# Performance work log

Hardware: AMD Instinct MI355X
Metric: run time of the kernel (lower is better)

## Reference

```python
import jax, jax.numpy as jnp
import numpy as np

H = 512  # hidden size

def _lstm_layer(xseq, W_ih, W_hh, b_ih, b_hh):
    """xseq: [S,B,D]. Returns (h_seq [S,B,H], c_final [B,H]). PyTorch gate order i,f,g,o."""
    S, B, _ = xseq.shape
    # precompute input contribution for all timesteps: [S,B,4H]
    gx = jnp.einsum('sbd,gd->sbg', xseq, W_ih) + b_ih + b_hh
    h0 = jnp.zeros((B, H), xseq.dtype)
    c0 = jnp.zeros((B, H), xseq.dtype)

    def step(carry, gx_t):
        h, c = carry
        gates = gx_t + h @ W_hh.T  # [B,4H]
        i, f, g, o = jnp.split(gates, 4, axis=-1)
        c = jax.nn.sigmoid(f) * c + jax.nn.sigmoid(i) * jnp.tanh(g)
        h = jax.nn.sigmoid(o) * jnp.tanh(c)
        return (h, c), h

    (_, c_fin), h_seq = jax.lax.scan(step, (h0, c0), gx)
    return h_seq, c_fin


def setup_inputs() -> dict:
    key = jax.random.key(0)
    ks = jax.random.split(key, 12)
    V, D, L = 50257, 300, 10
    s = 0.08  # weight scale to keep gates in a sane range
    return {
        'x': jax.random.randint(ks[0], (64, 512), 0, V),
        'emb': jax.random.normal(ks[1], (V, D), jnp.float32),
        'W_ih0': s * jax.random.normal(ks[2], (4 * H, D), jnp.float32),
        'W_hh0': s * jax.random.normal(ks[3], (4 * H, H), jnp.float32),
        'b_ih0': s * jax.random.normal(ks[4], (4 * H,), jnp.float32),
        'b_hh0': s * jax.random.normal(ks[5], (4 * H,), jnp.float32),
        'W_ih1': s * jax.random.normal(ks[6], (4 * H, H), jnp.float32),
        'W_hh1': s * jax.random.normal(ks[7], (4 * H, H), jnp.float32),
        'b_ih1': s * jax.random.normal(ks[8], (4 * H,), jnp.float32),
        'b_hh1': s * jax.random.normal(ks[9], (4 * H,), jnp.float32),
        'W_out': s * jax.random.normal(ks[10], (L, H), jnp.float32),
        'b_out': s * jax.random.normal(ks[11], (L,), jnp.float32),
    }


def reference(x, emb, W_ih0, W_hh0, b_ih0, b_hh0, W_ih1, W_hh1, b_ih1, b_hh1, W_out, b_out):
    xe = emb[x]                      # [B,S,D] embedding gather
    xe = jnp.transpose(xe, (1, 0, 2))  # [S,B,D] time-major for scan
    h1, _ = _lstm_layer(xe, W_ih0, W_hh0, b_ih0, b_hh0)
    _, c2 = _lstm_layer(h1, W_ih1, W_hh1, b_ih1, b_hh1)  # c_n[-1]: [B,H]
    return c2 @ W_out.T + b_out      # [B,n_labels]
```

## Files before the change

### kernel.cpp

```cpp
#include <hip/hip_runtime.h>
#include <hip/hip_bf16.h>
#include <stdint.h>

#define BB 64
#define SS 512
#define HH 512
#define DD 300
#define DP 320

typedef __attribute__((ext_vector_type(8))) short short8;
typedef __attribute__((ext_vector_type(4))) float f32x4;

__device__ __forceinline__ unsigned short f2bf(float f) {
  unsigned u = __builtin_bit_cast(unsigned, f);
  u += 0x7fffu + ((u >> 16) & 1u);
  return (unsigned short)(u >> 16);
}
__device__ __forceinline__ float sigm(float x) { return 1.f / (1.f + __expf(-x)); }
__device__ __forceinline__ float tanh_f(float x) {
  float t = __expf(-2.f * fabsf(x));
  float r = (1.f - t) / (1.f + t);
  return x < 0.f ? -r : r;
}

__device__ __forceinline__ short8 load_frag_sc1(const unsigned short* p) {
  short8 r;
  asm volatile("global_load_dwordx4 %0, %1, off sc1" : "=v"(r) : "v"(p));
  return r;
}
__device__ __forceinline__ short8 load_frag(const unsigned short* p) {
  short8 r;
  asm volatile("global_load_dwordx4 %0, %1, off" : "=v"(r) : "v"(p));
  return r;
}

#define OFF_ARR   0u
#define OFF_EP    8192u
#define OFF_H1    16384u
#define OFF_H2    147456u
#define OFF_C2    278528u
#define OFF_XE    409600u
#define OFF_W0    21381120u
#define OFF_W1    24788992u
#define OFF_B0    28983296u
#define OFF_B1    28991488u
#define MEMSET_BYTES 278528u

__global__ void prep_weights(const float* __restrict__ Wih0, const float* __restrict__ Whh0,
                             const float* __restrict__ bih0, const float* __restrict__ bhh0,
                             const float* __restrict__ Wih1, const float* __restrict__ Whh1,
                             const float* __restrict__ bih1, const float* __restrict__ bhh1,
                             unsigned short* __restrict__ Wp0, unsigned short* __restrict__ Wp1,
                             float* __restrict__ b0p, float* __restrict__ b1p)
{
  int idx = blockIdx.x * 256 + threadIdx.x;
  int grow = idx >> 10;
  int k1 = idx & 1023;
  int l = grow & 31;
  int lb = grow >> 5;
  int gate = l >> 3;
  int orig = gate * 512 + lb * 8 + (l & 7);
  float v1 = (k1 < 512) ? Wih1[orig * 512 + k1] : Whh1[orig * 512 + (k1 - 512)];
  Wp1[idx] = f2bf(v1);
  if (k1 < 832) {
    float v0;
    if (k1 < 512)      v0 = Whh0[orig * 512 + k1];
    else if (k1 < 812) v0 = Wih0[orig * 300 + (k1 - 512)];
    else               v0 = 0.f;
    Wp0[grow * 832 + k1] = f2bf(v0);
  }
  if (k1 == 0) {
    b0p[grow] = bih0[orig] + bhh0[orig];
    b1p[grow] = bih1[orig] + bhh1[orig];
  }
}

__global__ void gather_xe(const int* __restrict__ x, const float* __restrict__ emb,
                          unsigned short* __restrict__ xe)
{
  int idx = blockIdx.x * 256 + threadIdx.x;
  int dk = idx % DP;
  int rem = idx / DP;
  int b = rem % BB;
  int t = rem / BB;
  int tok = x[b * SS + t];
  float v = (dk < DD) ? emb[(size_t)tok * DD + dk] : 0.f;
  size_t ua = (size_t)t * 20480 + (size_t)(dk >> 5) * 2048 + (size_t)(b >> 4) * 512
            + (size_t)((dk >> 3) & 3) * 128 + (size_t)(b & 15) * 8 + (dk & 7);
  xe[ua] = f2bf(v);
}

template<bool IS_L0>
__device__ __forceinline__ void scan_body(
    int blk,
    const unsigned short* __restrict__ xe,
    const unsigned short* __restrict__ Wp,
    const float* __restrict__ biasP,
    unsigned short* __restrict__ h1r,
    unsigned short* __restrict__ h2r,
    float* __restrict__ c2,
    unsigned int* cnt,
    float (&gl)[2][64][36], float (&bias_sm)[32])
{
  constexpr int K  = IS_L0 ? 832 : 1024;
  constexpr int NK = IS_L0 ? 13 : 16;

  const int tid  = threadIdx.x;
  const int lane = tid & 63;
  const int wave = tid >> 6;
  const int lrow = lane & 15;
  const int m    = wave & 3;
  const int q    = wave >> 2;
  const int lblk = IS_L0 ? blk : blk - 64;
  const int qkb  = q * NK;

  if (tid < 32) bias_sm[tid] = biasP[lblk * 32 + tid];

  short8 Bf0[NK], Bf1[NK];
  {
    const unsigned short* wr0 = Wp + (size_t)(lblk * 32 + lrow) * K + qkb * 32 + (lane >> 4) * 8;
    const unsigned short* wr1 = wr0 + (size_t)16 * K;
    #pragma unroll
    for (int j = 0; j < NK; ++j) {
      Bf0[j] = *(const short8*)(wr0 + j * 32);
      Bf1[j] = *(const short8*)(wr1 + j * 32);
    }
  }
  #pragma unroll
  for (int j = 0; j < NK; ++j)
    asm volatile("" : "+v"(Bf0[j]), "+v"(Bf1[j]));

  float creg = 0.f;
  const int pb = tid >> 3;
  const int ph = tid & 7;
  const size_t hst = (size_t)(lblk >> 2) * 2048 + (size_t)(pb >> 4) * 512
                   + (size_t)(lblk & 3) * 128 + (size_t)(pb & 15) * 8 + ph;

  for (int k = 0;; ++k) {
    const bool active = IS_L0 ? (k < 512) : (k >= 1);
    short8 a[NK];

    if (IS_L0 && active) {
      const unsigned short* xet = xe + (size_t)k * 20480;
      #pragma unroll
      for (int j = 0; j < NK; ++j) {
        const int kg = qkb + j;
        if (kg >= 16)
          a[j] = load_frag(xet + (size_t)(kg - 16) * 2048 + (size_t)m * 512 + lane * 8);
      }
    }

    if (k >= 1) {
      if (wave == 0) {
        const unsigned tgt = (unsigned)k * 8u;
        int guard = 0;
        for (;;) {
          unsigned v = (lane < 16)
              ? __hip_atomic_load(cnt + lane * 128, __ATOMIC_RELAXED, __HIP_MEMORY_SCOPE_AGENT)
              : tgt;
          if (__all(v >= tgt)) break;
          if (++guard > (1 << 18)) break;
        }
      }
      __syncthreads();
    }

    if (active) {
      const int t = IS_L0 ? k : k - 1;
      const unsigned short* hA = h1r + (size_t)((IS_L0 ? (t + 1) : t) & 1) * 32768;
      const unsigned short* hB = h2r + (size_t)((t + 1) & 1) * 32768;

      #pragma unroll
      for (int j = 0; j < NK; ++j) {
        const int kg = qkb + j;
        if (kg < 16) {
          a[j] = load_frag_sc1(hA + (size_t)kg * 2048 + (size_t)m * 512 + lane * 8);
        } else if (!IS_L0) {
          a[j] = load_frag_sc1(hB + (size_t)(kg - 16) * 2048 + (size_t)m * 512 + lane * 8);
        }
      }
      asm volatile("s_waitcnt vmcnt(0)" ::: "memory");
      __builtin_amdgcn_sched_barrier(0);

      f32x4 acc0 = {0.f, 0.f, 0.f, 0.f};
      f32x4 acc1 = {0.f, 0.f, 0.f, 0.f};
      #pragma unroll
      for (int j = 0; j < NK; ++j) {
        acc0 = __builtin_amdgcn_mfma_f32_16x16x32_bf16(a[j], Bf0[j], acc0, 0, 0, 0);
        acc1 = __builtin_amdgcn_mfma_f32_16x16x32_bf16(a[j], Bf1[j], acc1, 0, 0, 0);
      }
      #pragma unroll
      for (int r = 0; r < 4; ++r) {
        const int bb = m * 16 + (lane >> 4) * 4 + r;
        gl[q][bb][lrow]      = acc0[r];
        gl[q][bb][16 + lrow] = acc1[r];
      }
      __syncthreads();

      {
        float gi = gl[0][pb][ph]      + gl[1][pb][ph]      + bias_sm[ph];
        float gf = gl[0][pb][8 + ph]  + gl[1][pb][8 + ph]  + bias_sm[8 + ph];
        float gg = gl[0][pb][16 + ph] + gl[1][pb][16 + ph] + bias_sm[16 + ph];
        float go = gl[0][pb][24 + ph] + gl[1][pb][24 + ph] + bias_sm[24 + ph];
        float iv = sigm(gi), fv = sigm(gf), ov = sigm(go), gv = tanh_f(gg);
        creg = fv * creg + iv * gv;
        float hv = ov * tanh_f(creg);
        unsigned short hb = f2bf(hv);
        unsigned pair = (unsigned)hb | ((unsigned)(unsigned short)__shfl_down((int)hb, 1) << 16);
        unsigned short* hw = (IS_L0 ? h1r : h2r) + (size_t)(t & 1) * 32768 + hst;
        if ((ph & 1) == 0)
          __hip_atomic_store((unsigned*)hw, pair, __ATOMIC_RELAXED, __HIP_MEMORY_SCOPE_AGENT);
        if (!IS_L0 && k == 512) c2[pb * HH + lblk * 8 + ph] = creg;
      }
      asm volatile("s_waitcnt vmcnt(0)" ::: "memory");
    }

    if (k == 512) break;
    __syncthreads();
    if (tid == 0)
      __hip_atomic_fetch_add(cnt + (blk >> 3) * 128, 1u, __ATOMIC_RELAXED,
                             __HIP_MEMORY_SCOPE_AGENT);
  }
}

__attribute__((amdgpu_waves_per_eu(2, 2)))
__global__ void __launch_bounds__(512)
lstm_scan(const unsigned short* __restrict__ xe,
          const unsigned short* __restrict__ Wp0,
          const unsigned short* __restrict__ Wp1,
          const float* __restrict__ b0p, const float* __restrict__ b1p,
          unsigned short* __restrict__ h1r, unsigned short* __restrict__ h2r,
          float* __restrict__ c2, unsigned int* __restrict__ cnt)
{
  __shared__ float gl[2][64][36];
  __shared__ float bias_sm[32];
  const int blk = blockIdx.x;
  if (blk < 64) scan_body<true >(blk, xe, Wp0, b0p, h1r, h2r, c2, cnt, gl, bias_sm);
  else          scan_body<false>(blk, xe, Wp1, b1p, h1r, h2r, c2, cnt, gl, bias_sm);
}

__global__ void outproj(const float* __restrict__ c2, const float* __restrict__ Wout,
                        const float* __restrict__ bout, float* __restrict__ out)
{
  int t = threadIdx.x;
  if (t >= 640) return;
  int b = t / 10, l = t % 10;
  float s = bout[l];
  #pragma unroll 8
  for (int h = 0; h < 512; ++h) s += c2[b * 512 + h] * Wout[l * 512 + h];
  out[b * 10 + l] = s;
}

extern "C" void kernel_launch(void* const* d_in, const int* in_sizes, int n_in,
                              void* d_out, int out_size, void* d_ws, size_t ws_size,
                              hipStream_t stream) {
  (void)in_sizes; (void)n_in; (void)out_size; (void)ws_size;
  const int*   x    = (const int*)  d_in[0];
  const float* emb  = (const float*)d_in[1];
  const float* Wih0 = (const float*)d_in[2];
  const float* Whh0 = (const float*)d_in[3];
  const float* bih0 = (const float*)d_in[4];
  const float* bhh0 = (const float*)d_in[5];
  const float* Wih1 = (const float*)d_in[6];
  const float* Whh1 = (const float*)d_in[7];
  const float* bih1 = (const float*)d_in[8];
  const float* bhh1 = (const float*)d_in[9];
  const float* Wout = (const float*)d_in[10];
  const float* bout = (const float*)d_in[11];
  float* out = (float*)d_out;

  char* ws = (char*)d_ws;
  unsigned int*   cnt = (unsigned int*)  (ws + OFF_ARR);
  unsigned short* h1r = (unsigned short*)(ws + OFF_H1);
  unsigned short* h2r = (unsigned short*)(ws + OFF_H2);
  float*          c2  = (float*)         (ws + OFF_C2);
  unsigned short* xe  = (unsigned short*)(ws + OFF_XE);
  unsigned short* Wp0 = (unsigned short*)(ws + OFF_W0);
  unsigned short* Wp1 = (unsigned short*)(ws + OFF_W1);
  float*          b0p = (float*)         (ws + OFF_B0);
  float*          b1p = (float*)         (ws + OFF_B1);

  hipMemsetAsync(ws, 0, MEMSET_BYTES, stream);
  prep_weights<<<8192, 256, 0, stream>>>(Wih0, Whh0, bih0, bhh0, Wih1, Whh1, bih1, bhh1,
                                         Wp0, Wp1, b0p, b1p);
  gather_xe<<<40960, 256, 0, stream>>>(x, emb, xe);
  lstm_scan<<<128, 512, 0, stream>>>(xe, Wp0, Wp1, b0p, b1p, h1r, h2r, c2, cnt);
  outproj<<<1, 640, 0, stream>>>(c2, Wout, bout, out);
}
```

Baseline: 2.240 ms.

## Fuse both LSTM layers into each block and use per-block sequence flags

Each of 64 persistent blocks now computes its 32 gate rows for both layer 0 and layer 1 in the same timestep, instead of 128 blocks split by layer. Cross-block synchronisation changes from shared atomic counters to per-block sequence numbers that each block stores and every block polls, with s_sleep added in the poll loop. Weights are no longer held in registers; they are reloaded from global memory every step, presumably because the larger per-block footprint would not fit. This halves the number of participating blocks and simplifies the barrier, but it adds per-step weight traffic through cache and doubles the MFMA work per block.

Result: slower. 8.404 ms (+275.2%).

```diff
diff --git a/kernel.cpp b/kernel.cpp
--- a/kernel.cpp
+++ b/kernel.cpp
@@ -23,28 +23,33 @@
   return x < 0.f ? -r : r;
 }
 
+__device__ __forceinline__ short8 load_frag(const unsigned short* p) {
+  short8 r;
+  asm volatile("global_load_dwordx4 %0, %1, off" : "=v"(r) : "v"(p));
+  return r;
+}
 __device__ __forceinline__ short8 load_frag_sc1(const unsigned short* p) {
   short8 r;
   asm volatile("global_load_dwordx4 %0, %1, off sc1" : "=v"(r) : "v"(p));
   return r;
 }
-__device__ __forceinline__ short8 load_frag(const unsigned short* p) {
-  short8 r;
-  asm volatile("global_load_dwordx4 %0, %1, off" : "=v"(r) : "v"(p));
-  return r;
-}
-
-#define OFF_ARR   0u
-#define OFF_EP    8192u
-#define OFF_H1    16384u
-#define OFF_H2    147456u
-#define OFF_C2    278528u
-#define OFF_XE    409600u
-#define OFF_W0    21381120u
-#define OFF_W1    24788992u
-#define OFF_B0    28983296u
-#define OFF_B1    28991488u
-#define MEMSET_BYTES 278528u
+__device__ __forceinline__ unsigned ld_seq(const unsigned int* p) {
+  return __hip_atomic_load(p, __ATOMIC_RELAXED, __HIP_MEMORY_SCOPE_AGENT);
+}
+__device__ __forceinline__ void st_seq(unsigned int* p, unsigned v) {
+  __hip_atomic_store(p, v, __ATOMIC_RELAXED, __HIP_MEMORY_SCOPE_AGENT);
+}
+
+#define OFF_SEQ   0u
+#define OFF_H1    8192u
+#define OFF_H2    139264u
+#define OFF_C2    270336u
+#define OFF_XE    401408u
+#define OFF_W0    21372928u
+#define OFF_W1    24780800u
+#define OFF_B0    28975104u
+#define OFF_B1    28983296u
+#define MEMSET_BYTES 270336u
 
 __global__ void prep_weights(const float* __restrict__ Wih0, const float* __restrict__ Whh0,
                              const float* __restrict__ bih0, const float* __restrict__ bhh0,
@@ -90,139 +95,6 @@
   xe[ua] = f2bf(v);
 }
 
-template<bool IS_L0>
-__device__ __forceinline__ void scan_body(
-    int blk,
-    const unsigned short* __restrict__ xe,
-    const unsigned short* __restrict__ Wp,
-    const float* __restrict__ biasP,
-    unsigned short* __restrict__ h1r,
-    unsigned short* __restrict__ h2r,
-    float* __restrict__ c2,
-    unsigned int* cnt,
-    float (&gl)[2][64][36], float (&bias_sm)[32])
-{
-  constexpr int K  = IS_L0 ? 832 : 1024;
-  constexpr int NK = IS_L0 ? 13 : 16;
-
-  const int tid  = threadIdx.x;
-  const int lane = tid & 63;
-  const int wave = tid >> 6;
-  const int lrow = lane & 15;
-  const int m    = wave & 3;
-  const int q    = wave >> 2;
-  const int lblk = IS_L0 ? blk : blk - 64;
-  const int qkb  = q * NK;
-
-  if (tid < 32) bias_sm[tid] = biasP[lblk * 32 + tid];
-
-  short8 Bf0[NK], Bf1[NK];
-  {
-    const unsigned short* wr0 = Wp + (size_t)(lblk * 32 + lrow) * K + qkb * 32 + (lane >> 4) * 8;
-    const unsigned short* wr1 = wr0 + (size_t)16 * K;
-    #pragma unroll
-    for (int j = 0; j < NK; ++j) {
-      Bf0[j] = *(const short8*)(wr0 + j * 32);
-      Bf1[j] = *(const short8*)(wr1 + j * 32);
-    }
-  }
-  #pragma unroll
-  for (int j = 0; j < NK; ++j)
-    asm volatile("" : "+v"(Bf0[j]), "+v"(Bf1[j]));
-
-  float creg = 0.f;
-  const int pb = tid >> 3;
-  const int ph = tid & 7;
-  const size_t hst = (size_t)(lblk >> 2) * 2048 + (size_t)(pb >> 4) * 512
-                   + (size_t)(lblk & 3) * 128 + (size_t)(pb & 15) * 8 + ph;
-
-  for (int k = 0;; ++k) {
-    const bool active = IS_L0 ? (k < 512) : (k >= 1);
-    short8 a[NK];
-
-    if (IS_L0 && active) {
-      const unsigned short* xet = xe + (size_t)k * 20480;
-      #pragma unroll
-      for (int j = 0; j < NK; ++j) {
-        const int kg = qkb + j;
-        if (kg >= 16)
-          a[j] = load_frag(xet + (size_t)(kg - 16) * 2048 + (size_t)m * 512 + lane * 8);
-      }
-    }
-
-    if (k >= 1) {
-      if (wave == 0) {
-        const unsigned tgt = (unsigned)k * 8u;
-        int guard = 0;
-        for (;;) {
-          unsigned v = (lane < 16)
-              ? __hip_atomic_load(cnt + lane * 128, __ATOMIC_RELAXED, __HIP_MEMORY_SCOPE_AGENT)
-              : tgt;
-          if (__all(v >= tgt)) break;
-          if (++guard > (1 << 18)) break;
-        }
-      }
-      __syncthreads();
-    }
-
-    if (active) {
-      const int t = IS_L0 ? k : k - 1;
-      const unsigned short* hA = h1r + (size_t)((IS_L0 ? (t + 1) : t) & 1) * 32768;
-      const unsigned short* hB = h2r + (size_t)((t + 1) & 1) * 32768;
-
-      #pragma unroll
-      for (int j = 0; j < NK; ++j) {
-        const int kg = qkb + j;
-        if (kg < 16) {
-          a[j] = load_frag_sc1(hA + (size_t)kg * 2048 + (size_t)m * 512 + lane * 8);
-        } else if (!IS_L0) {
-          a[j] = load_frag_sc1(hB + (size_t)(kg - 16) * 2048 + (size_t)m * 512 + lane * 8);
-        }
-      }
-      asm volatile("s_waitcnt vmcnt(0)" ::: "memory");
-      __builtin_amdgcn_sched_barrier(0);
-
-      f32x4 acc0 = {0.f, 0.f, 0.f, 0.f};
-      f32x4 acc1 = {0.f, 0.f, 0.f, 0.f};
-      #pragma unroll
-      for (int j = 0; j < NK; ++j) {
-        acc0 = __builtin_amdgcn_mfma_f32_16x16x32_bf16(a[j], Bf0[j], acc0, 0, 0, 0);
-        acc1 = __builtin_amdgcn_mfma_f32_16x16x32_bf16(a[j], Bf1[j], acc1, 0, 0, 0);
-      }
-      #pragma unroll
-      for (int r = 0; r < 4; ++r) {
-        const int bb = m * 16 + (lane >> 4) * 4 + r;
-        gl[q][bb][lrow]      = acc0[r];
-        gl[q][bb][16 + lrow] = acc1[r];
-      }
-      __syncthreads();
-
-      {
-        float gi = gl[0][pb][ph]      + gl[1][pb][ph]      + bias_sm[ph];
-        float gf = gl[0][pb][8 + ph]  + gl[1][pb][8 + ph]  + bias_sm[8 + ph];
-        float gg = gl[0][pb][16 + ph] + gl[1][pb][16 + ph] + bias_sm[16 + ph];
-        float go = gl[0][pb][24 + ph] + gl[1][pb][24 + ph] + bias_sm[24 + ph];
-        float iv = sigm(gi), fv = sigm(gf), ov = sigm(go), gv = tanh_f(gg);
-        creg = fv * creg + iv * gv;
-        float hv = ov * tanh_f(creg);
-        unsigned short hb = f2bf(hv);
-        unsigned pair = (unsigned)hb | ((unsigned)(unsigned short)__shfl_down((int)hb, 1) << 16);
-        unsigned short* hw = (IS_L0 ? h1r : h2r) + (size_t)(t & 1) * 32768 + hst;
-        if ((ph & 1) == 0)
-          __hip_atomic_store((unsigned*)hw, pair, __ATOMIC_RELAXED, __HIP_MEMORY_SCOPE_AGENT);
-        if (!IS_L0 && k == 512) c2[pb * HH + lblk * 8 + ph] = creg;
-      }
-      asm volatile("s_waitcnt vmcnt(0)" ::: "memory");
-    }
-
-    if (k == 512) break;
-    __syncthreads();
-    if (tid == 0)
-      __hip_atomic_fetch_add(cnt + (blk >> 3) * 128, 1u, __ATOMIC_RELAXED,
-                             __HIP_MEMORY_SCOPE_AGENT);
-  }
-}
-
 __attribute__((amdgpu_waves_per_eu(2, 2)))
 __global__ void __launch_bounds__(512)
 lstm_scan(const unsigned short* __restrict__ xe,
@@ -230,13 +102,150 @@
           const unsigned short* __restrict__ Wp1,
           const float* __restrict__ b0p, const float* __restrict__ b1p,
           unsigned short* __restrict__ h1r, unsigned short* __restrict__ h2r,
-          float* __restrict__ c2, unsigned int* __restrict__ cnt)
-{
-  __shared__ float gl[2][64][36];
-  __shared__ float bias_sm[32];
-  const int blk = blockIdx.x;
-  if (blk < 64) scan_body<true >(blk, xe, Wp0, b0p, h1r, h2r, c2, cnt, gl, bias_sm);
-  else          scan_body<false>(blk, xe, Wp1, b1p, h1r, h2r, c2, cnt, gl, bias_sm);
+          float* __restrict__ c2, unsigned int* __restrict__ seq)
+{
+  __shared__ float gl0[2][64][36];
+  __shared__ float gl1[2][64][36];
+  __shared__ float bias0_sm[32], bias1_sm[32];
+
+  const int lblk = blockIdx.x;
+  const int tid  = threadIdx.x;
+  const int lane = tid & 63;
+  const int wave = tid >> 6;
+  const int lrow = lane & 15;
+  const int m    = wave & 3;
+  const int q    = wave >> 2;
+
+  if (tid < 32)       bias0_sm[tid]      = b0p[lblk * 32 + tid];
+  else if (tid < 64)  bias1_sm[tid - 32] = b1p[lblk * 32 + (tid - 32)];
+
+  const unsigned short* w0a = Wp0 + (size_t)(lblk * 32 + lrow) * 832 + (q ? 512 : 0)
+                            + (lane >> 4) * 8;
+  const unsigned short* w0b = w0a + (size_t)16 * 832;
+  const unsigned short* w1a = Wp1 + (size_t)(lblk * 32 + lrow) * 1024 + q * 512
+                            + (lane >> 4) * 8;
+  const unsigned short* w1b = w1a + (size_t)16 * 1024;
+  const int NL0 = q ? 10 : 16;
+
+  float c1reg = 0.f, c2reg = 0.f;
+  const int pb = tid >> 3;
+  const int ph = tid & 7;
+  const size_t hstu = (size_t)(lblk >> 2) * 2048 + (size_t)(pb >> 4) * 512
+                    + (size_t)(lblk & 3) * 128 + (size_t)(pb & 15) * 8 + ph;
+
+  for (int t = 0; t <= 512; ++t) {
+    short8 axe[10];
+    if (q == 1) {
+      const int tx = (t < 512) ? t : 511;
+      const unsigned short* xet = xe + (size_t)tx * 20480;
+      #pragma unroll
+      for (int j = 0; j < 10; ++j)
+        axe[j] = load_frag(xet + (size_t)j * 2048 + (size_t)m * 512 + lane * 8);
+    }
+
+    if (t >= 1) {
+      if (wave == 0) {
+        int guard = 0;
+        for (;;) {
+          unsigned v = ld_seq(seq + lane * 16);
+          if (__all(v >= (unsigned)t)) break;
+          if (++guard > (1 << 18)) break;
+          __builtin_amdgcn_s_sleep(1);
+        }
+      }
+    }
+    __syncthreads();
+
+    short8 ah[16];
+    if (q == 0) {
+      const unsigned short* hA = h1r + (size_t)((t + 1) & 1) * 32768;
+      #pragma unroll
+      for (int j = 0; j < 16; ++j)
+        ah[j] = load_frag_sc1(hA + (size_t)j * 2048 + (size_t)m * 512 + lane * 8);
+    } else {
+      const unsigned short* hB = h2r + (size_t)(t & 1) * 32768;
+      #pragma unroll
+      for (int j = 0; j < 16; ++j)
+        ah[j] = load_frag_sc1(hB + (size_t)j * 2048 + (size_t)m * 512 + lane * 8);
+    }
+    asm volatile("s_waitcnt vmcnt(0)" ::: "memory");
+    __builtin_amdgcn_sched_barrier(0);
+
+    f32x4 a00 = {0.f,0.f,0.f,0.f}, a01 = {0.f,0.f,0.f,0.f};
+    f32x4 a10 = {0.f,0.f,0.f,0.f}, a11 = {0.f,0.f,0.f,0.f};
+    if (q == 0) {
+      #pragma unroll
+      for (int j = 0; j < 16; ++j) {
+        short8 b0 = *(const short8*)(w0a + j * 32);
+        short8 b1 = *(const short8*)(w0b + j * 32);
+        short8 b2 = *(const short8*)(w1a + j * 32);
+        short8 b3 = *(const short8*)(w1b + j * 32);
+        a00 = __builtin_amdgcn_mfma_f32_16x16x32_bf16(ah[j], b0, a00, 0, 0, 0);
+        a01 = __builtin_amdgcn_mfma_f32_16x16x32_bf16(ah[j], b1, a01, 0, 0, 0);
+        a10 = __builtin_amdgcn_mfma_f32_16x16x32_bf16(ah[j], b2, a10, 0, 0, 0);
+        a11 = __builtin_amdgcn_mfma_f32_16x16x32_bf16(ah[j], b3, a11, 0, 0, 0);
+      }
+    } else {
+      #pragma unroll
+      for (int j = 0; j < 10; ++j) {
+        short8 b0 = *(const short8*)(w0a + j * 32);
+        short8 b1 = *(const short8*)(w0b + j * 32);
+        a00 = __builtin_amdgcn_mfma_f32_16x16x32_bf16(axe[j], b0, a00, 0, 0, 0);
+        a01 = __builtin_amdgcn_mfma_f32_16x16x32_bf16(axe[j], b1, a01, 0, 0, 0);
+      }
+      #pragma unroll
+      for (int j = 0; j < 16; ++j) {
+        short8 b2 = *(const short8*)(w1a + j * 32);
+        short8 b3 = *(const short8*)(w1b + j * 32);
+        a10 = __builtin_amdgcn_mfma_f32_16x16x32_bf16(ah[j], b2, a10, 0, 0, 0);
+        a11 = __builtin_amdgcn_mfma_f32_16x16x32_bf16(ah[j], b3, a11, 0, 0, 0);
+      }
+    }
+    #pragma unroll
+    for (int r = 0; r < 4; ++r) {
+      const int bb = m * 16 + (lane >> 4) * 4 + r;
+      gl0[q][bb][lrow]      = a00[r];
+      gl0[q][bb][16 + lrow] = a01[r];
+      gl1[q][bb][lrow]      = a10[r];
+      gl1[q][bb][16 + lrow] = a11[r];
+    }
+    __syncthreads();
+
+    if (t < 512) {
+      const float* g0 = gl0[0][pb];
+      const float* g1 = gl0[1][pb];
+      float gi = g0[ph]      + g1[ph]      + bias0_sm[ph];
+      float gf = g0[8 + ph]  + g1[8 + ph]  + bias0_sm[8 + ph];
+      float gg = g0[16 + ph] + g1[16 + ph] + bias0_sm[16 + ph];
+      float go = g0[24 + ph] + g1[24 + ph] + bias0_sm[24 + ph];
+      float iv = sigm(gi), fv = sigm(gf), ov = sigm(go), gv = tanh_f(gg);
+      c1reg = fv * c1reg + iv * gv;
+      float hv = ov * tanh_f(c1reg);
+      unsigned short hb = f2bf(hv);
+      unsigned pair = (unsigned)hb | ((unsigned)(unsigned short)__shfl_down((int)hb, 1) << 16);
+      if ((ph & 1) == 0)
+        st_seq((unsigned*)(h1r + (size_t)(t & 1) * 32768 + hstu), pair);
+    }
+    if (t >= 1) {
+      const float* g0 = gl1[0][pb];
+      const float* g1 = gl1[1][pb];
+      float gi = g0[ph]      + g1[ph]      + bias1_sm[ph];
+      float gf = g0[8 + ph]  + g1[8 + ph]  + bias1_sm[8 + ph];
+      float gg = g0[16 + ph] + g1[16 + ph] + bias1_sm[16 + ph];
+      float go = g0[24 + ph] + g1[24 + ph] + bias1_sm[24 + ph];
+      float iv = sigm(gi), fv = sigm(gf), ov = sigm(go), gv = tanh_f(gg);
+      c2reg = fv * c2reg + iv * gv;
+      float hv = ov * tanh_f(c2reg);
+      unsigned short hb = f2bf(hv);
+      unsigned pair = (unsigned)hb | ((unsigned)(unsigned short)__shfl_down((int)hb, 1) << 16);
+      if ((ph & 1) == 0)
+        st_seq((unsigned*)(h2r + (size_t)((t + 1) & 1) * 32768 + hstu), pair);
+      if (t == 512) c2[pb * HH + lblk * 8 + ph] = c2reg;
+    }
+    asm volatile("s_waitcnt vmcnt(0)" ::: "memory");
+    __syncthreads();
+    if (tid == 0 && t < 512) st_seq(seq + lblk * 16, (unsigned)(t + 1));
+  }
 }
 
 __global__ void outproj(const float* __restrict__ c2, const float* __restrict__ Wout,
@@ -270,20 +279,20 @@
   float* out = (float*)d_out;
 
   char* ws = (char*)d_ws;
-  unsigned int*   cnt = (unsigned int*)  (ws + OFF_ARR);
-  unsigned short* h1r = (unsigned short*)(ws + OFF_H1);
-  unsigned short* h2r = (unsigned short*)(ws + OFF_H2);
-  float*          c2  = (float*)         (ws + OFF_C2);
-  unsigned short* xe  = (unsigned short*)(ws + OFF_XE);
-  unsigned short* Wp0 = (unsigned short*)(ws + OFF_W0);
-  unsigned short* Wp1 = (unsigned short*)(ws + OFF_W1);
-  float*          b0p = (float*)         (ws + OFF_B0);
-  float*          b1p = (float*)         (ws + OFF_B1);
+  unsigned int*   seqb = (unsigned int*)  (ws + OFF_SEQ);
+  unsigned short* h1r  = (unsigned short*)(ws + OFF_H1);
+  unsigned short* h2r  = (unsigned short*)(ws + OFF_H2);
+  float*          c2   = (float*)         (ws + OFF_C2);
+  unsigned short* xe   = (unsigned short*)(ws + OFF_XE);
+  unsigned short* Wp0  = (unsigned short*)(ws + OFF_W0);
+  unsigned short* Wp1  = (unsigned short*)(ws + OFF_W1);
+  float*          b0p  = (float*)         (ws + OFF_B0);
+  float*          b1p  = (float*)         (ws + OFF_B1);
 
   hipMemsetAsync(ws, 0, MEMSET_BYTES, stream);
   prep_weights<<<8192, 256, 0, stream>>>(Wih0, Whh0, bih0, bhh0, Wih1, Whh1, bih1, bhh1,
                                          Wp0, Wp1, b0p, b1p);
   gather_xe<<<40960, 256, 0, stream>>>(x, emb, xe);
-  lstm_scan<<<128, 512, 0, stream>>>(xe, Wp0, Wp1, b0p, b1p, h1r, h2r, c2, cnt);
+  lstm_scan<<<64, 512, 0, stream>>>(xe, Wp0, Wp1, b0p, b1p, h1r, h2r, c2, seqb);
   outproj<<<1, 640, 0, stream>>>(c2, Wout, bout, out);
 }
```
